# Kernel tuning notes

Measured on AMD Instinct MI355X. Metric: run time of the kernel, lower is better.

## Reference

```python
import jax, jax.numpy as jnp
import numpy as np

COST_CLASS = 1.0
COST_BBOX = 1.0
COST_GIOU = 1.0
NUM_TGT_PER_IMG = 100  # sizes[b] for every image (equal-size, padded-batch style)


def box_cxcywh_to_xyxy(b):
    cx, cy, w, h = jnp.split(b, 4, axis=-1)
    return jnp.concatenate([cx - 0.5 * w, cy - 0.5 * h, cx + 0.5 * w, cy + 0.5 * h], axis=-1)


def generalized_box_iou(b1, b2):
    # b1: [N,4], b2: [M,4] in xyxy -> [N,M]
    area1 = (b1[:, 2] - b1[:, 0]) * (b1[:, 3] - b1[:, 1])
    area2 = (b2[:, 2] - b2[:, 0]) * (b2[:, 3] - b2[:, 1])
    lt = jnp.maximum(b1[:, None, :2], b2[None, :, :2])
    rb = jnp.minimum(b1[:, None, 2:], b2[None, :, 2:])
    wh = jnp.clip(rb - lt, 0.0)
    inter = wh[..., 0] * wh[..., 1]
    union = area1[:, None] + area2[None, :] - inter
    iou = inter / union
    lt_e = jnp.minimum(b1[:, None, :2], b2[None, :, :2])
    rb_e = jnp.maximum(b1[:, None, 2:], b2[None, :, 2:])
    wh_e = jnp.clip(rb_e - lt_e, 0.0)
    area_e = wh_e[..., 0] * wh_e[..., 1]
    return iou - (area_e - union) / area_e


def build_cost_matrix(logits, pred_boxes, tgt_labels, tgt_boxes):
    B, Q, C = logits.shape
    out_prob = jax.nn.sigmoid(logits).reshape(B * Q, C)        # [BQ, C]
    out_bbox = pred_boxes.reshape(B * Q, 4)                     # [BQ, 4]
    tgt_ids = tgt_labels.reshape(-1)                            # [BT]
    tgt_bbox = tgt_boxes.reshape(-1, 4)                         # [BT, 4]
    cost_class = -out_prob[:, tgt_ids]                          # [BQ, BT]
    cost_bbox = jnp.sum(jnp.abs(out_bbox[:, None, :] - tgt_bbox[None, :, :]), axis=-1)  # L1 cdist
    cost_giou = -generalized_box_iou(box_cxcywh_to_xyxy(out_bbox), box_cxcywh_to_xyxy(tgt_bbox))
    cost = COST_BBOX * cost_bbox + COST_CLASS * cost_class + COST_GIOU * cost_giou
    return cost.reshape(B, Q, -1)                               # [B, Q, B*T]


def greedy_match(cost, curr_targets):
    # Faithful to _greedy_matcher: iteratively pick the globally smallest-cost
    # unmatched (row, col) pair among columns < curr_targets. Equivalent to the
    # stable-sorted flat scan (argmin breaks ties at lowest flat index, matching
    # the stable ascending sort).
    Q, Ttot = cost.shape
    col_ok = jnp.arange(Ttot) < curr_targets
    c0 = jnp.where(col_ok[None, :], cost, jnp.inf)
    num_match = min(Q, curr_targets)

    def step(c, _):
        idx = jnp.argmin(c.reshape(-1))
        r = idx // Ttot
        col = idx % Ttot
        c = c.at[r, :].set(jnp.inf).at[:, col].set(jnp.inf)
        return c, (r.astype(jnp.int32), col.astype(jnp.int32))

    _, (rows, cols) = jax.lax.scan(step, c0, None, length=num_match)
    return rows, cols


def setup_inputs() -> dict:
    key = jax.random.key(0)
    k1, k2, k3, k4, k5, k6 = jax.random.split(key, 6)
    B, Q, C, T = 16, 900, 91, NUM_TGT_PER_IMG
    logits = jax.random.normal(k1, (B, Q, C), dtype=jnp.float32)
    pb_cxcy = jax.random.uniform(k2, (B, Q, 2), dtype=jnp.float32)
    pb_wh = jax.random.uniform(k3, (B, Q, 2), dtype=jnp.float32, minval=0.05, maxval=0.5)
    pred_boxes = jnp.concatenate([pb_cxcy, pb_wh], axis=-1)
    tgt_labels = jax.random.randint(k4, (B, T), 0, C)
    tb_cxcy = jax.random.uniform(k5, (B, T, 2), dtype=jnp.float32)
    tb_wh = jax.random.uniform(k6, (B, T, 2), dtype=jnp.float32, minval=0.05, maxval=0.5)
    tgt_boxes = jnp.concatenate([tb_cxcy, tb_wh], axis=-1)
    return {"logits": logits, "pred_boxes": pred_boxes, "tgt_labels": tgt_labels, "tgt_boxes": tgt_boxes}


def reference(logits, pred_boxes, tgt_labels, tgt_boxes):
    cost = build_cost_matrix(logits, pred_boxes, tgt_labels, tgt_boxes)  # [B, Q, B*T]
    rows, cols = jax.vmap(lambda c: greedy_match(c, NUM_TGT_PER_IMG))(cost)
    return cost, rows, cols
```

## Files before the change

kernel.cpp:

```cpp
#include <hip/hip_runtime.h>
#include <math.h>

#define BB 16
#define QQ 900
#define CC 91
#define TT 100
#define BT (BB * TT)
#define NTHREADS 256
#define TILE 15
#define NBLK_PER_IMG (QQ / TILE)
#define NSLOT 15
#define WSCOLS 128

__device__ __forceinline__ unsigned ordkey(float f) {
    unsigned u = __float_as_uint(f);
    return (u & 0x80000000u) ? ~u : (u | 0x80000000u);
}

__device__ __forceinline__ unsigned long long u64min(unsigned long long a, unsigned long long b) {
    return a < b ? a : b;
}

__device__ __forceinline__ unsigned long long packkrc(unsigned key, int row, int col) {
    return ((unsigned long long)key << 21) | ((unsigned long long)row << 11) | (unsigned)col;
}

__global__ __launch_bounds__(NTHREADS) void cost_kernel(
    const float* __restrict__ logits,
    const float* __restrict__ pred,
    const int*   __restrict__ tlab,
    const float* __restrict__ tbox,
    float*       __restrict__ cost,
    unsigned long long* __restrict__ colmin)
{
    const int b  = blockIdx.x / NBLK_PER_IMG;
    const int tb = blockIdx.x % NBLK_PER_IMG;
    const int r0 = tb * TILE;

    __shared__ float s_tx[BT], s_ty[BT], s_tz[BT], s_tw[BT];
    __shared__ int   s_lab[BT];
    __shared__ float s_sig[TILE][CC];
    __shared__ float s_row[TILE][8];
    __shared__ float s_cmin[TILE][TT];

    for (int j = threadIdx.x; j < BT; j += NTHREADS) {
        float4 t = *(const float4*)(tbox + (size_t)j * 4);
        s_tx[j] = t.x; s_ty[j] = t.y; s_tz[j] = t.z; s_tw[j] = t.w;
        s_lab[j] = tlab[j];
    }
    for (int u = threadIdx.x; u < TILE * CC; u += NTHREADS) {
        int r = u / CC, c = u % CC;
        float x = logits[((size_t)(b * QQ + r0 + r)) * CC + c];
        s_sig[r][c] = 1.0f / (1.0f + expf(-x));
    }
    if (threadIdx.x < TILE) {
        int r = threadIdx.x;
        const float4 p = *(const float4*)(pred + ((size_t)(b * QQ + r0 + r)) * 4);
        s_row[r][0] = p.x; s_row[r][1] = p.y; s_row[r][2] = p.z; s_row[r][3] = p.w;
        s_row[r][4] = p.x - 0.5f * p.z;
        s_row[r][5] = p.y - 0.5f * p.w;
        s_row[r][6] = p.x + 0.5f * p.z;
        s_row[r][7] = p.y + 0.5f * p.w;
    }
    __syncthreads();

    for (int r = 0; r < TILE; ++r) {
        const float px  = s_row[r][0], py  = s_row[r][1], pz  = s_row[r][2], pw  = s_row[r][3];
        const float p_x0 = s_row[r][4], p_y0 = s_row[r][5], p_x1 = s_row[r][6], p_y1 = s_row[r][7];
        const float area1 = (p_x1 - p_x0) * (p_y1 - p_y0);
        float* crow = cost + ((size_t)(b * QQ + r0 + r)) * BT;

        for (int j = threadIdx.x; j < BT; j += NTHREADS) {
            float tx = s_tx[j], ty = s_ty[j], tz = s_tz[j], tw = s_tw[j];
            float cclass = -s_sig[r][s_lab[j]];
            float cbbox = ((fabsf(px - tx) + fabsf(py - ty)) + fabsf(pz - tz)) + fabsf(pw - tw);

            float t_x0 = tx - 0.5f * tz, t_y0 = ty - 0.5f * tw;
            float t_x1 = tx + 0.5f * tz, t_y1 = ty + 0.5f * tw;
            float area2 = (t_x1 - t_x0) * (t_y1 - t_y0);

            float ltx = fmaxf(p_x0, t_x0), lty = fmaxf(p_y0, t_y0);
            float rbx = fminf(p_x1, t_x1), rby = fminf(p_y1, t_y1);
            float iw = fmaxf(rbx - ltx, 0.0f), ih = fmaxf(rby - lty, 0.0f);
            float inter = iw * ih;
            float uni = (area1 + area2) - inter;
            float iou = inter / uni;

            float ex0 = fminf(p_x0, t_x0), ey0 = fminf(p_y0, t_y0);
            float ex1 = fmaxf(p_x1, t_x1), ey1 = fmaxf(p_y1, t_y1);
            float ew = fmaxf(ex1 - ex0, 0.0f), eh = fmaxf(ey1 - ey0, 0.0f);
            float ae = ew * eh;
            float giou = iou - (ae - uni) / ae;

            float v = (cbbox + cclass) + (-giou);
            crow[j] = v;
            if (j < TT) s_cmin[r][j] = v;
        }
    }
    __syncthreads();

    if (threadIdx.x < TT) {
        const int c = threadIdx.x;
        unsigned long long best = ~0ULL;
        #pragma unroll
        for (int r = 0; r < TILE; ++r)
            best = u64min(best, packkrc(ordkey(s_cmin[r][c]), r0 + r, c));
        atomicMin(colmin + (size_t)b * WSCOLS + c, best);
    }
}

__global__ __launch_bounds__(64, 1) void greedy_kernel(
    const float* __restrict__ cost,
    const unsigned long long* __restrict__ colmin,
    float*       __restrict__ rows_out,
    float*       __restrict__ cols_out)
{
    const int b = blockIdx.x;
    const int lane = threadIdx.x;
    const float* cb = cost + (size_t)b * QQ * BT;

    unsigned long long cola = colmin[(size_t)b * WSCOLS + lane];
    unsigned long long colb = (lane < TT - 64)
                            ? colmin[(size_t)b * WSCOLS + 64 + lane] : ~0ULL;

    unsigned rowok = (lane < 4) ? 0x7FFFu : 0x3FFFu;

    for (int step = 0; step < TT; ++step) {
        unsigned long long m = u64min(cola, colb);
        #pragma unroll
        for (int off = 1; off < 64; off <<= 1)
            m = u64min(m, __shfl_xor(m, off, 64));

        const int rstar = (int)((m >> 11) & 0x3FF);
        const int cstar = (int)(m & 0x7FF);

        if (lane == 0) {
            rows_out[b * TT + step] = (float)rstar;
            cols_out[b * TT + step] = (float)cstar;
        }

        if (lane == cstar)        cola = ~0ULL;
        if (lane + 64 == cstar)   colb = ~0ULL;
        if (lane == (rstar & 63)) rowok &= ~(1u << (rstar >> 6));

        unsigned long long hitsA = __ballot((int)((cola >> 11) & 0x3FF) == rstar);
        unsigned long long hitsB = __ballot((int)((colb >> 11) & 0x3FF) == rstar);

        while (hitsA | hitsB) {
            int c;
            if (hitsA) { c = (int)__ffsll((unsigned long long)hitsA) - 1;      hitsA &= hitsA - 1; }
            else       { c = (int)__ffsll((unsigned long long)hitsB) - 1 + 64; hitsB &= hitsB - 1; }

            unsigned long long best = ~0ULL;
            #pragma unroll
            for (int i = 0; i < NSLOT; ++i) {
                if ((rowok >> i) & 1u) {
                    const int r = i * 64 + lane;
                    float v = cb[(size_t)r * BT + c];
                    best = u64min(best, packkrc(ordkey(v), r, c));
                }
            }
            #pragma unroll
            for (int off = 1; off < 64; off <<= 1)
                best = u64min(best, __shfl_xor(best, off, 64));

            if (lane == c)      cola = best;
            if (lane + 64 == c) colb = best;
        }
    }
}

extern "C" void kernel_launch(void* const* d_in, const int* in_sizes, int n_in,
                              void* d_out, int out_size, void* d_ws, size_t ws_size,
                              hipStream_t stream) {
    const float* logits = (const float*)d_in[0];
    const float* pred   = (const float*)d_in[1];
    const int*   tlab   = (const int*)d_in[2];
    const float* tbox   = (const float*)d_in[3];

    float* out = (float*)d_out;
    float* cost = out;
    float* rows = out + (size_t)BB * QQ * BT;
    float* cols = rows + (size_t)BB * TT;

    unsigned long long* colmin = (unsigned long long*)d_ws;

    hipMemsetAsync(d_ws, 0xFF, (size_t)BB * WSCOLS * sizeof(unsigned long long), stream);

    cost_kernel<<<BB * NBLK_PER_IMG, NTHREADS, 0, stream>>>(logits, pred, tlab, tbox, cost, colmin);
    greedy_kernel<<<BB, 64, 0, stream>>>(cost, colmin, rows, cols);
}
```

Baseline: 226.2 us.

## Sort column minima once and lazily rescan stale columns in greedy matcher

The greedy matcher now bitonic-sorts the per-column minima across the wavefront once. It then walks them in order, using a small pending buffer of rescanned column minima, so each step needs no full wave reduction and only a popped entry whose row is already taken triggers a column rescan. The cost kernel also reduces column minima in registers instead of going through shared memory, which removes a barrier. The risk is the fixed 8-entry pending buffer: if more than 8 rescanned columns are pending at once, an entry is silently dropped and the matching becomes incorrect.

```diff
diff --git a/kernel.cpp b/kernel.cpp
--- a/kernel.cpp
+++ b/kernel.cpp
@@ -11,6 +11,7 @@
 #define NBLK_PER_IMG (QQ / TILE)
 #define NSLOT 15
 #define WSCOLS 128
+#define PENDK 8
 
 __device__ __forceinline__ unsigned ordkey(float f) {
     unsigned u = __float_as_uint(f);
@@ -20,9 +21,18 @@
 __device__ __forceinline__ unsigned long long u64min(unsigned long long a, unsigned long long b) {
     return a < b ? a : b;
 }
+__device__ __forceinline__ unsigned long long u64max(unsigned long long a, unsigned long long b) {
+    return a > b ? a : b;
+}
 
 __device__ __forceinline__ unsigned long long packkrc(unsigned key, int row, int col) {
     return ((unsigned long long)key << 21) | ((unsigned long long)row << 11) | (unsigned)col;
+}
+
+__device__ __forceinline__ unsigned long long rdlane64(unsigned long long v, int l) {
+    unsigned lo = (unsigned)__builtin_amdgcn_readlane((int)(unsigned)v, l);
+    unsigned hi = (unsigned)__builtin_amdgcn_readlane((int)(unsigned)(v >> 32), l);
+    return ((unsigned long long)hi << 32) | lo;
 }
 
 __global__ __launch_bounds__(NTHREADS) void cost_kernel(
@@ -41,7 +51,6 @@
     __shared__ int   s_lab[BT];
     __shared__ float s_sig[TILE][CC];
     __shared__ float s_row[TILE][8];
-    __shared__ float s_cmin[TILE][TT];
 
     for (int j = threadIdx.x; j < BT; j += NTHREADS) {
         float4 t = *(const float4*)(tbox + (size_t)j * 4);
@@ -64,6 +73,8 @@
     }
     __syncthreads();
 
+    unsigned long long bestc = ~0ULL;
+
     for (int r = 0; r < TILE; ++r) {
         const float px  = s_row[r][0], py  = s_row[r][1], pz  = s_row[r][2], pw  = s_row[r][3];
         const float p_x0 = s_row[r][4], p_y0 = s_row[r][5], p_x1 = s_row[r][6], p_y1 = s_row[r][7];
@@ -94,19 +105,12 @@
 
             float v = (cbbox + cclass) + (-giou);
             crow[j] = v;
-            if (j < TT) s_cmin[r][j] = v;
-        }
-    }
-    __syncthreads();
-
-    if (threadIdx.x < TT) {
-        const int c = threadIdx.x;
-        unsigned long long best = ~0ULL;
-        #pragma unroll
-        for (int r = 0; r < TILE; ++r)
-            best = u64min(best, packkrc(ordkey(s_cmin[r][c]), r0 + r, c));
-        atomicMin(colmin + (size_t)b * WSCOLS + c, best);
-    }
+            if (j < TT) bestc = u64min(bestc, packkrc(ordkey(v), r0 + r, j));
+        }
+    }
+
+    if (threadIdx.x < TT)
+        atomicMin(colmin + (size_t)b * WSCOLS + threadIdx.x, bestc);
 }
 
 __global__ __launch_bounds__(64, 1) void greedy_kernel(
@@ -119,53 +123,89 @@
     const int lane = threadIdx.x;
     const float* cb = cost + (size_t)b * QQ * BT;
 
-    unsigned long long cola = colmin[(size_t)b * WSCOLS + lane];
-    unsigned long long colb = (lane < TT - 64)
-                            ? colmin[(size_t)b * WSCOLS + 64 + lane] : ~0ULL;
+    unsigned long long va = colmin[(size_t)b * WSCOLS + lane];
+    unsigned long long vb = (lane < TT - 64)
+                          ? colmin[(size_t)b * WSCOLS + 64 + lane] : ~0ULL;
+
+    #pragma unroll
+    for (int k = 2; k <= 128; k <<= 1) {
+        #pragma unroll
+        for (int j = k >> 1; j > 0; j >>= 1) {
+            if (j == 64) {
+                unsigned long long lo = u64min(va, vb);
+                unsigned long long hi = va ^ vb ^ lo;
+                va = lo; vb = hi;
+            } else {
+                unsigned long long pa = __shfl_xor(va, j, 64);
+                bool ta = ((lane & j) == 0) == ((lane & k) == 0);
+                va = ta ? u64min(va, pa) : u64max(va, pa);
+                unsigned long long pb = __shfl_xor(vb, j, 64);
+                int ib = lane + 64;
+                bool tb_ = ((ib & j) == 0) == ((ib & k) == 0);
+                vb = tb_ ? u64min(vb, pb) : u64max(vb, pb);
+            }
+        }
+    }
 
     unsigned rowok = (lane < 4) ? 0x7FFFu : 0x3FFFu;
-
-    for (int step = 0; step < TT; ++step) {
-        unsigned long long m = u64min(cola, colb);
-        #pragma unroll
-        for (int off = 1; off < 64; off <<= 1)
-            m = u64min(m, __shfl_xor(m, off, 64));
-
-        const int rstar = (int)((m >> 11) & 0x3FF);
-        const int cstar = (int)(m & 0x7FF);
-
-        if (lane == 0) {
-            rows_out[b * TT + step] = (float)rstar;
-            cols_out[b * TT + step] = (float)cstar;
-        }
-
-        if (lane == cstar)        cola = ~0ULL;
-        if (lane + 64 == cstar)   colb = ~0ULL;
-        if (lane == (rstar & 63)) rowok &= ~(1u << (rstar >> 6));
-
-        unsigned long long hitsA = __ballot((int)((cola >> 11) & 0x3FF) == rstar);
-        unsigned long long hitsB = __ballot((int)((colb >> 11) & 0x3FF) == rstar);
-
-        while (hitsA | hitsB) {
-            int c;
-            if (hitsA) { c = (int)__ffsll((unsigned long long)hitsA) - 1;      hitsA &= hitsA - 1; }
-            else       { c = (int)__ffsll((unsigned long long)hitsB) - 1 + 64; hitsB &= hitsB - 1; }
-
+    unsigned long long pend[PENDK];
+    #pragma unroll
+    for (int t = 0; t < PENDK; ++t) pend[t] = ~0ULL;
+    unsigned long long pmin = ~0ULL;
+
+    int p = 0;
+    int match = 0;
+    while (match < TT) {
+        unsigned long long s = (p < 64) ? rdlane64(va, p)
+                             : (p < 128) ? rdlane64(vb, p - 64) : ~0ULL;
+        bool fromPend = pmin < s;
+        unsigned long long e = fromPend ? pmin : s;
+
+        const int rstar = (int)((e >> 11) & 0x3FF);
+        const int cstar = (int)(e & 0x7FF);
+
+        bool alive = __ballot((lane == (rstar & 63)) && ((rowok >> (rstar >> 6)) & 1u)) != 0ULL;
+
+        if (fromPend) {
+            bool removed = false;
+            #pragma unroll
+            for (int t = 0; t < PENDK; ++t) {
+                if (!removed && pend[t] == e) { pend[t] = ~0ULL; removed = true; }
+            }
+            pmin = ~0ULL;
+            #pragma unroll
+            for (int t = 0; t < PENDK; ++t) pmin = u64min(pmin, pend[t]);
+        } else {
+            ++p;
+        }
+
+        if (alive) {
+            if (lane == 0) {
+                rows_out[b * TT + match] = (float)rstar;
+                cols_out[b * TT + match] = (float)cstar;
+            }
+            if (lane == (rstar & 63)) rowok &= ~(1u << (rstar >> 6));
+            ++match;
+        } else {
             unsigned long long best = ~0ULL;
             #pragma unroll
             for (int i = 0; i < NSLOT; ++i) {
                 if ((rowok >> i) & 1u) {
                     const int r = i * 64 + lane;
-                    float v = cb[(size_t)r * BT + c];
-                    best = u64min(best, packkrc(ordkey(v), r, c));
+                    float v = cb[(size_t)r * BT + cstar];
+                    best = u64min(best, packkrc(ordkey(v), r, cstar));
                 }
             }
             #pragma unroll
             for (int off = 1; off < 64; off <<= 1)
                 best = u64min(best, __shfl_xor(best, off, 64));
 
-            if (lane == c)      cola = best;
-            if (lane + 64 == c) colb = best;
+            bool placed = false;
+            #pragma unroll
+            for (int t = 0; t < PENDK; ++t) {
+                if (!placed && pend[t] == ~0ULL) { pend[t] = best; placed = true; }
+            }
+            pmin = u64min(pmin, best);
         }
     }
 }
```

After: 204.7 us. -9.5%, faster.
